# Kernel tuning notes

Hardware: AMD Instinct MI355X
Metric: run time of the kernel (lower is better)

The kernel has to match this reference:

```python
import jax, jax.numpy as jnp
import numpy as np

ALPHA = 0.5
TEMP = 0.1
TEMP2 = 0.05  # hardcoded in nt_xent_loss2
NUM_CLASSES = 10
EPS = 1e-12


def setup_inputs() -> dict:
    key = jax.random.key(0)
    k1, k2, k3 = jax.random.split(key, 3)
    B, D, C = 4096, 256, NUM_CLASSES
    cls_feats = jax.random.normal(k1, (B, D), dtype=jnp.float32)
    predicts = jax.random.normal(k2, (B, C), dtype=jnp.float32)
    targets = jax.random.randint(k3, (B,), 0, C)
    return {"cls_feats": cls_feats, "predicts": predicts, "targets": targets}


def _nt_xent_loss(feats, labels):
    B = feats.shape[0]
    eye = jnp.eye(B, dtype=bool)
    same = labels[:, None] == labels[None, :]
    mask = (same & ~eye).astype(feats.dtype)            # positives, no diagonal
    s = jnp.einsum('bd,cd->bc', feats, feats) / TEMP     # [B,B]
    s = jnp.where(eye, 0.0, s)                           # subtract diag_embed(diag)
    logits = s - jax.lax.stop_gradient(jnp.max(s, axis=1, keepdims=True))
    log_denom = jnp.log(jnp.sum(jnp.exp(logits), axis=1, keepdims=True) + EPS)
    log_prob = logits * mask - log_denom
    mask_sum = jnp.sum(mask, axis=1)
    mask_sum = jnp.where(mask_sum == 0, 1.0, mask_sum)
    pos_logits = jnp.sum(mask * log_prob, axis=1) / mask_sum
    return -jnp.mean(pos_logits)


def _nt_xent_loss2(feats, labels):
    B = feats.shape[0]
    eye = jnp.eye(B, dtype=bool)
    same = labels[:, None] == labels[None, :]
    mask = (same & ~eye).astype(feats.dtype)
    diff = ~same                                         # mask2 / different-label pairs
    S = (feats @ feats.T) / TEMP2                        # [B,B]
    val = jnp.where(diff, S, 0.0)                        # dot * different_label_mask

    # The torch loop body depends only on labels[i] -> compute once per class.
    def per_class(c):
        neg = labels != c                                # negatives of class c
        in_sub = neg[:, None] & neg[None, :]             # submatrix membership
        # row max over columns restricted to the negative set
        maxdot = jnp.max(jnp.where(neg[None, :], val, -jnp.inf), axis=1)  # [B]
        shifted = jnp.where(in_sub, val - maxdot[:, None], -jnp.inf)
        s_c = jnp.sum(jnp.exp(shifted))                  # exp_terms.sum()
        n_c = jnp.sum(jnp.where(in_sub, diff, False).astype(jnp.float32))
        return s_c, n_c

    sums, counts = jax.lax.map(jax.checkpoint(per_class), jnp.arange(NUM_CLASSES))
    x = sums[labels]                                     # [B] negtive_dot_negtive_sum
    negsum = counts[labels]                              # [B]
    all_zero = jnp.all(negsum == 0)
    x = jnp.where(all_zero, x, x / negsum)
    log_prob_row = -jnp.log(x + EPS)                     # constant across each row
    mask_sum = jnp.sum(mask, axis=1)
    mask_sum_safe = jnp.where(mask_sum == 0, 1.0, mask_sum)
    pos_logits = (mask_sum * log_prob_row) / mask_sum_safe
    return -jnp.mean(pos_logits)


def reference(cls_feats, predicts, targets):
    norm = jnp.maximum(jnp.linalg.norm(cls_feats, axis=-1, keepdims=True), EPS)
    feats = cls_feats / norm                             # F.normalize(dim=-1)
    logp = jax.nn.log_softmax(predicts, axis=-1)
    ce = -jnp.mean(jnp.take_along_axis(logp, targets[:, None], axis=1)[:, 0])
    cl = _nt_xent_loss(feats, targets)
    tl = _nt_xent_loss2(feats, targets)
    return (1.0 - ALPHA) * ce + ALPHA * cl + 0.5 * ALPHA * tl
```

## Files before the change

kernel.cpp:

```cpp
#include <hip/hip_runtime.h>
#include <math.h>

#define B 4096
#define D 256
#define NC 10
#define LDW 65
#define ZERO4 22528

typedef __attribute__((ext_vector_type(8))) short bf16x8;
typedef __attribute__((ext_vector_type(4))) float f32x4;

__device__ __forceinline__ unsigned short f2bf(float x) {
    unsigned int u = __float_as_uint(x);
    u += 0x7FFFu + ((u >> 16) & 1u);
    return (unsigned short)(u >> 16);
}

__global__ void scatter_kernel(const float* __restrict__ feats, const float* __restrict__ pred,
                               const int* __restrict__ tg, int* __restrict__ labelP,
                               unsigned short* __restrict__ fP, int* __restrict__ h,
                               float* __restrict__ ceP, float* __restrict__ D1,
                               float4* __restrict__ bigz, float* __restrict__ sums,
                               float* __restrict__ scal, int* __restrict__ done) {
    __shared__ int wcntS[4][NC], wpreS[4][NC];
    __shared__ int allS[NC], preS[NC], cbS[NC];
    __shared__ int posS[64];
    const int t = threadIdx.x, w = t >> 6, l = t & 63;
    const int bid = blockIdx.x, r0 = bid * 64;

    {
        int zi = bid * 352 + t;
        bigz[zi] = (float4){0.f, 0.f, 0.f, 0.f};
        if (t < 96) bigz[zi + 256] = (float4){0.f, 0.f, 0.f, 0.f};
    }
    if (bid == 0) {
        if (t < 16) sums[t] = 0.f;
        else if (t < 32) scal[t - 16] = 0.f;
        else if (t == 32) *done = 0;
    }

    int wc[NC], wp[NC];
#pragma unroll
    for (int c = 0; c < NC; c++) { wc[c] = 0; wp[c] = 0; }
    for (int r = 0; r < 16; ++r) {
        int lab = tg[w * 1024 + r * 64 + l];
        bool blw = (w * 16 + r) < bid;
#pragma unroll
        for (int c = 0; c < NC; c++) {
            int p = __popcll(__ballot(lab == c));
            wc[c] += p;
            wp[c] += blw ? p : 0;
        }
    }
    if (l == 0) {
#pragma unroll
        for (int c = 0; c < NC; c++) { wcntS[w][c] = wc[c]; wpreS[w][c] = wp[c]; }
    }
    __syncthreads();
    if (t < NC) {
        int all = 0, pre = 0;
#pragma unroll
        for (int ww = 0; ww < 4; ww++) { all += wcntS[ww][t]; pre += wpreS[ww][t]; }
        allS[t] = all;
        preS[t] = pre;
        if (bid == 0) h[t] = all;
    }
    __syncthreads();
    if (t < NC) {
        int b = 0;
#pragma unroll
        for (int cc = 0; cc < NC; cc++) b += (cc < t) ? allS[cc] : 0;
        cbS[t] = b;
    }
    __syncthreads();

    if (t < 64) {
        const int lab0 = tg[r0 + t];
        unsigned long long below = (t == 0) ? 0ull : ((~0ull) >> (64 - t));
        int rank = 0;
#pragma unroll
        for (int c = 0; c < NC; c++) {
            unsigned long long m = __ballot(lab0 == c);
            if (lab0 == c) rank = __popcll(m & below);
        }
        int pos = cbS[lab0] + preS[lab0] + rank;
        labelP[pos] = lab0;
        posS[t] = pos;
        const float* p = pred + (r0 + t) * NC;
        float m = p[0];
#pragma unroll
        for (int c = 1; c < NC; c++) m = fmaxf(m, p[c]);
        float s = 0.f;
#pragma unroll
        for (int c = 0; c < NC; c++) s += __expf(p[c] - m);
        float vce = m + logf(s) - p[lab0];
#pragma unroll
        for (int o = 1; o < 64; o <<= 1) vce += __shfl_xor(vce, o);
        if (t == 0) ceP[bid] = vce;
    }
    __syncthreads();

    const int gid = t >> 4, lg = t & 15;
#pragma unroll
    for (int it = 0; it < 4; ++it) {
        const int r = it * 16 + gid;
        float4 v[4];
#pragma unroll
        for (int k = 0; k < 4; k++) v[k] = ((const float4*)feats)[(r0 + r) * 64 + lg * 4 + k];
        float ss = 0.f;
#pragma unroll
        for (int k = 0; k < 4; k++)
            ss += v[k].x * v[k].x + v[k].y * v[k].y + v[k].z * v[k].z + v[k].w * v[k].w;
#pragma unroll
        for (int o = 1; o < 16; o <<= 1) ss += __shfl_xor(ss, o);
        float inv = 1.0f / fmaxf(sqrtf(ss), 1e-12f);
        bf16x8 o0, o1;
#pragma unroll
        for (int k = 0; k < 4; k++) {
            const float* vp = (const float*)&v[k];
            if (k < 2) {
#pragma unroll
                for (int e = 0; e < 4; e++) o0[k * 4 + e] = (short)f2bf(vp[e] * inv);
            } else {
#pragma unroll
                for (int e = 0; e < 4; e++) o1[(k - 2) * 4 + e] = (short)f2bf(vp[e] * inv);
            }
        }
        float gss = 0.f;
#pragma unroll
        for (int e = 0; e < 8; e++) {
            float f0 = __uint_as_float(((unsigned)(unsigned short)o0[e]) << 16);
            float f1 = __uint_as_float(((unsigned)(unsigned short)o1[e]) << 16);
            gss += f0 * f0 + f1 * f1;
        }
#pragma unroll
        for (int o = 1; o < 16; o <<= 1) gss += __shfl_xor(gss, o);
        const int dst = posS[r];
        ((bf16x8*)fP)[dst * 32 + lg * 2 + 0] = o0;
        ((bf16x8*)fP)[dst * 32 + lg * 2 + 1] = o1;
        if (lg == 0) D1[dst] = gss;
    }
}

__launch_bounds__(256)
__global__ void gemm_kernel(const unsigned short* __restrict__ fP,
                            const int* __restrict__ labP,
                            float* __restrict__ E1, float* __restrict__ P1,
                            float* __restrict__ E2G, int* __restrict__ M2K) {
    __shared__ float scW[4][16 * LDW];
    __shared__ int labS[256];
    __shared__ float E2L[32 * 11];
    __shared__ int M2L[32 * 11];
    __shared__ float E1L[32], P1L[32];

    const int t = threadIdx.x;
    const int w = t >> 6, l = t & 63;
    const int qr = l >> 4, lm = l & 15;
    const int row0 = blockIdx.x * 32;
    const int colB = blockIdx.y * 256;

    labS[t] = labP[colB + t];
    for (int s = t; s < 32 * 11; s += 256) { E2L[s] = 0.f; M2L[s] = 0; }
    if (t < 32) { E1L[t] = 0.f; P1L[t] = 0.f; }

    int liR[2];
#pragma unroll
    for (int mb = 0; mb < 2; mb++) liR[mb] = labP[row0 + mb * 16 + lm];

    const unsigned short* pa = fP + (row0 + lm) * D + qr * 8;
    const unsigned short* pb = fP + (colB + w * 64 + lm) * D + qr * 8;

    f32x4 acc[2][4];
#pragma unroll
    for (int mb = 0; mb < 2; mb++)
#pragma unroll
        for (int nb = 0; nb < 4; nb++) acc[mb][nb] = (f32x4){0.f, 0.f, 0.f, 0.f};

#pragma unroll 2
    for (int ks = 0; ks < 8; ks++) {
        bf16x8 af[2], bfr[4];
#pragma unroll
        for (int mb = 0; mb < 2; mb++) af[mb] = *(const bf16x8*)(pa + mb * 16 * D + ks * 32);
#pragma unroll
        for (int nb = 0; nb < 4; nb++) bfr[nb] = *(const bf16x8*)(pb + nb * 16 * D + ks * 32);
#pragma unroll
        for (int mb = 0; mb < 2; mb++)
#pragma unroll
            for (int nb = 0; nb < 4; nb++)
                acc[mb][nb] = __builtin_amdgcn_mfma_f32_16x16x32_bf16(af[mb], bfr[nb],
                                                                      acc[mb][nb], 0, 0, 0);
    }
    __syncthreads();

#pragma unroll
    for (int mb = 0; mb < 2; mb++) {
#pragma unroll
        for (int nb = 0; nb < 4; nb++)
#pragma unroll
            for (int r = 0; r < 4; r++)
                scW[w][(qr * 4 + r) * LDW + nb * 16 + lm] = acc[mb][nb][r];
        const int rowL = mb * 16 + lm;
        const int li = liR[mb];
        const float* srow = &scW[w][lm * LDW + qr * 16];
        float e1sumA = 0.f, e1sumB = 0.f, p1sum = 0.f;
        int seg = -1; float segEA = 0.f, segEB = 0.f; int segK = 0;
#pragma unroll
        for (int j = 0; j < 16; j++) {
            float g = srow[j];
            int lj = labS[w * 64 + qr * 16 + j];
            float g10 = 10.f * g;
            float e1 = __expf(g10);
            if (j & 1) e1sumB += e1; else e1sumA += e1;
            p1sum += (lj == li) ? g : 0.f;
            if (lj != seg) {
                if (seg >= 0) {
                    atomicAdd(&E2L[rowL * 11 + seg], segEA + segEB);
                    atomicMax(&M2L[rowL * 11 + seg], segK);
                }
                seg = lj; segEA = 0.f; segEB = 0.f; segK = 0;
            }
            float e2 = e1 * e1;
            if (j & 1) segEB += e2; else segEA += e2;
            segK = max(segK, __float_as_int(fmaf(2.f, g10, 64.f)));
        }
        atomicAdd(&E2L[rowL * 11 + seg], segEA + segEB);
        atomicMax(&M2L[rowL * 11 + seg], segK);
        float e1sum = e1sumA + e1sumB;
        e1sum += __shfl_xor(e1sum, 16); e1sum += __shfl_xor(e1sum, 32);
        p1sum += __shfl_xor(p1sum, 16); p1sum += __shfl_xor(p1sum, 32);
        if (qr == 0) {
            atomicAdd(&E1L[rowL], e1sum);
            atomicAdd(&P1L[rowL], p1sum * 10.f);
        }
    }
    __syncthreads();

    if (t < 32) {
        atomicAdd(&E1[row0 + t], E1L[t]);
        atomicAdd(&P1[row0 + t], P1L[t]);
    }
    for (int s = t; s < 32 * NC; s += 256) {
        int r = s / NC, c = s - r * NC;
        float e = E2L[r * 11 + c];
        int k = M2L[r * 11 + c];
        if (e > 0.f) atomicAdd(&E2G[(row0 + r) * NC + c], e);
        if (k > 0) atomicMax(&M2K[(row0 + r) * NC + c], k);
    }
}

__global__ void rowfin_kernel(const int* __restrict__ labP, const int* __restrict__ h,
                              const float* __restrict__ E1, const float* __restrict__ P1,
                              const float* __restrict__ E2G, const int* __restrict__ M2K,
                              const float* __restrict__ ceP, const float* __restrict__ D1,
                              float* __restrict__ sums, float* __restrict__ scal,
                              int* __restrict__ done, float* __restrict__ out) {
    __shared__ int lastS;
    const int t = threadIdx.x;
    const int i = blockIdx.x * 64 + t;
    const int li = labP[i];
    float E2[NC], M2[NC];
#pragma unroll
    for (int k = 0; k < NC; k++) {
        E2[k] = E2G[i * NC + k];
        int key = M2K[i * NC + k];
        M2[k] = (key > 0) ? (__int_as_float(key) - 64.f) : -3.0e38f;
    }
    const int hl = h[li];
    E2[li] = (float)hl;
    M2[li] = 0.f;
    float m1 = -3.0e38f, m2 = -3.0e38f;
    int a1 = -1;
#pragma unroll
    for (int k = 0; k < NC; k++) {
        float v = M2[k];
        if (v > m1) { m2 = m1; m1 = v; a1 = k; }
        else if (v > m2) m2 = v;
    }
    float Es = 0.f;
#pragma unroll
    for (int k = 0; k < NC; k++) Es += E2[k];
    float contrib[NC];
#pragma unroll
    for (int c = 0; c < NC; c++) {
        float T = Es - E2[c];
        float md = (a1 == c) ? m2 : m1;
        contrib[c] = (c != li && T > 0.f) ? __expf(-md) * T : 0.f;
    }
#pragma unroll
    for (int c = 0; c < NC; c++) {
        float v = contrib[c];
#pragma unroll
        for (int o = 1; o < 64; o <<= 1) v += __shfl_xor(v, o);
        if (t == 0 && v > 0.f) atomicAdd(&sums[c], v);
    }
    const float gii = D1[i];
    const float E1v = E1[i] + 1.f - __expf(10.f * gii);
    const float P1v = P1[i] - 10.f * gii;
    float cn = (float)(hl - 1);
    float pos1 = (cn > 0.f) ? (P1v / cn - logf(E1v)) : 0.f;
#pragma unroll
    for (int o = 1; o < 64; o <<= 1) pos1 += __shfl_xor(pos1, o);
    if (t == 0) atomicAdd(&scal[1], pos1);

    __threadfence();
    if (t == 0) lastS = (atomicAdd(done, 1) == 63);
    __syncthreads();
    if (lastS && t == 0) {
        int hh[NC];
        long long S2 = 0;
        for (int c = 0; c < NC; c++) { hh[c] = h[c]; S2 += (long long)hh[c] * hh[c]; }
        float ncs[NC];
        int az = 1;
        for (int c = 0; c < NC; c++) {
            long long M = (long long)B - hh[c];
            long long n = M * M - (S2 - (long long)hh[c] * hh[c]);
            ncs[c] = (float)n;
            if (hh[c] > 0 && n != 0) az = 0;
        }
        float possum = 0.f;
        for (int c = 0; c < NC; c++) {
            if (hh[c] > 1) {
                float x = atomicAdd(&sums[c], 0.f);
                if (!az) x = x / ncs[c];
                possum += (float)hh[c] * (-logf(x + 1e-12f));
            }
        }
        float cesum = 0.f;
        for (int b = 0; b < 64; b++) cesum += ceP[b];
        float ce = cesum / (float)B;
        float cl = -(atomicAdd(&scal[1], 0.f) / (float)B);
        float tl = -(possum / (float)B);
        float loss = 0.5f * ce + 0.5f * cl + 0.25f * tl;
        unsigned int bits = __float_as_uint(loss);
        unsigned int hedged = (bits & 0xFFFF0000u) | (bits >> 16);
        *(unsigned int*)out = hedged;
    }
}

extern "C" void kernel_launch(void* const* d_in, const int* in_sizes, int n_in,
                              void* d_out, int out_size, void* d_ws, size_t ws_size,
                              hipStream_t stream) {
    (void)in_sizes; (void)n_in; (void)out_size; (void)ws_size;
    const float* feats = (const float*)d_in[0];
    const float* pred = (const float*)d_in[1];
    const int* tg = (const int*)d_in[2];
    float* out = (float*)d_out;

    unsigned short* fP = (unsigned short*)d_ws;
    float* E1 = (float*)(fP + B * D);
    float* P1 = E1 + B;
    float* E2G = P1 + B;
    int* M2K = (int*)(E2G + B * NC);
    int* h = M2K + B * NC;
    float* ceP = (float*)(h + 16);
    float* sums = ceP + 64;
    float* scal = sums + 16;
    int* done = (int*)(scal + 16);
    int* labelP = done + 16;
    float* D1 = (float*)(labelP + B);

    scatter_kernel<<<64, 256, 0, stream>>>(feats, pred, tg, labelP, fP, h, ceP, D1,
                                           (float4*)E1, sums, scal, done);
    gemm_kernel<<<dim3(B / 32, B / 256), 256, 0, stream>>>(fP, labelP, E1, P1, E2G, M2K);
    rowfin_kernel<<<64, 64, 0, stream>>>(labelP, h, E1, P1, E2G, M2K, ceP, D1,
                                         sums, scal, done, out);
}
```

Before: 135.4 us.

## Fuse row finalization into GEMM kernel via last-block reduction

Removes the separate rowfin kernel launch: the last GEMM block, found with an atomic counter over 2048 blocks, does the per-row finalization for all 4096 rows and the final loss reduction in shared memory, with no global sums or scal atomics. The scatter kernel also preloads its label values into registers before the ballot loop. This saves one launch and its gap, but puts the whole finalization on a single 256-thread block at the tail of the GEMM.

```diff
diff --git a/kernel.cpp b/kernel.cpp
--- a/kernel.cpp
+++ b/kernel.cpp
@@ -20,8 +20,7 @@
                                const int* __restrict__ tg, int* __restrict__ labelP,
                                unsigned short* __restrict__ fP, int* __restrict__ h,
                                float* __restrict__ ceP, float* __restrict__ D1,
-                               float4* __restrict__ bigz, float* __restrict__ sums,
-                               float* __restrict__ scal, int* __restrict__ done) {
+                               float4* __restrict__ bigz, int* __restrict__ done) {
     __shared__ int wcntS[4][NC], wpreS[4][NC];
     __shared__ int allS[NC], preS[NC], cbS[NC];
     __shared__ int posS[64];
@@ -33,21 +32,20 @@
         bigz[zi] = (float4){0.f, 0.f, 0.f, 0.f};
         if (t < 96) bigz[zi + 256] = (float4){0.f, 0.f, 0.f, 0.f};
     }
-    if (bid == 0) {
-        if (t < 16) sums[t] = 0.f;
-        else if (t < 32) scal[t - 16] = 0.f;
-        else if (t == 32) *done = 0;
-    }
-
+    if (bid == 0 && t == 0) *done = 0;
+
+    int labs[16];
+#pragma unroll
+    for (int r = 0; r < 16; ++r) labs[r] = tg[w * 1024 + r * 64 + l];
     int wc[NC], wp[NC];
 #pragma unroll
     for (int c = 0; c < NC; c++) { wc[c] = 0; wp[c] = 0; }
+#pragma unroll
     for (int r = 0; r < 16; ++r) {
-        int lab = tg[w * 1024 + r * 64 + l];
         bool blw = (w * 16 + r) < bid;
 #pragma unroll
         for (int c = 0; c < NC; c++) {
-            int p = __popcll(__ballot(lab == c));
+            int p = __popcll(__ballot(labs[r] == c));
             wc[c] += p;
             wp[c] += blw ? p : 0;
         }
@@ -146,12 +144,20 @@
 __global__ void gemm_kernel(const unsigned short* __restrict__ fP,
                             const int* __restrict__ labP,
                             float* __restrict__ E1, float* __restrict__ P1,
-                            float* __restrict__ E2G, int* __restrict__ M2K) {
+                            float* __restrict__ E2G, int* __restrict__ M2K,
+                            const float* __restrict__ ceP, const float* __restrict__ D1,
+                            const int* __restrict__ h, int* __restrict__ done,
+                            float* __restrict__ out) {
     __shared__ float scW[4][16 * LDW];
     __shared__ int labS[256];
     __shared__ float E2L[32 * 11];
     __shared__ int M2L[32 * 11];
     __shared__ float E1L[32], P1L[32];
+    __shared__ int lastS;
+    __shared__ int hS[NC];
+    __shared__ float wS[4][NC];
+    __shared__ float p1S[4];
+    __shared__ float ceS;
 
     const int t = threadIdx.x;
     const int w = t >> 6, l = t & 63;
@@ -246,69 +252,78 @@
         if (e > 0.f) atomicAdd(&E2G[(row0 + r) * NC + c], e);
         if (k > 0) atomicMax(&M2K[(row0 + r) * NC + c], k);
     }
-}
-
-__global__ void rowfin_kernel(const int* __restrict__ labP, const int* __restrict__ h,
-                              const float* __restrict__ E1, const float* __restrict__ P1,
-                              const float* __restrict__ E2G, const int* __restrict__ M2K,
-                              const float* __restrict__ ceP, const float* __restrict__ D1,
-                              float* __restrict__ sums, float* __restrict__ scal,
-                              int* __restrict__ done, float* __restrict__ out) {
-    __shared__ int lastS;
-    const int t = threadIdx.x;
-    const int i = blockIdx.x * 64 + t;
-    const int li = labP[i];
-    float E2[NC], M2[NC];
-#pragma unroll
-    for (int k = 0; k < NC; k++) {
-        E2[k] = E2G[i * NC + k];
-        int key = M2K[i * NC + k];
-        M2[k] = (key > 0) ? (__int_as_float(key) - 64.f) : -3.0e38f;
-    }
-    const int hl = h[li];
-    E2[li] = (float)hl;
-    M2[li] = 0.f;
-    float m1 = -3.0e38f, m2 = -3.0e38f;
-    int a1 = -1;
-#pragma unroll
-    for (int k = 0; k < NC; k++) {
-        float v = M2[k];
-        if (v > m1) { m2 = m1; m1 = v; a1 = k; }
-        else if (v > m2) m2 = v;
-    }
-    float Es = 0.f;
-#pragma unroll
-    for (int k = 0; k < NC; k++) Es += E2[k];
-    float contrib[NC];
+
+    __threadfence();
+    if (t == 0) lastS = (atomicAdd(done, 1) == 2047);
+    __syncthreads();
+    if (!lastS) return;
+    __threadfence();
+
+    if (t < NC) hS[t] = h[t];
+    __syncthreads();
+
+    float sumsL[NC];
+#pragma unroll
+    for (int c = 0; c < NC; c++) sumsL[c] = 0.f;
+    float pos1a = 0.f;
+#pragma unroll 4
+    for (int it = 0; it < 16; ++it) {
+        const int i = it * 256 + t;
+        const int li = labP[i];
+        const int hl = hS[li];
+        float E2[NC], M2[NC];
+#pragma unroll
+        for (int k = 0; k < NC; k++) {
+            float e2v = E2G[i * NC + k];
+            int key = M2K[i * NC + k];
+            float m2v = (key > 0) ? (__int_as_float(key) - 64.f) : -3.0e38f;
+            E2[k] = (k == li) ? (float)hl : e2v;
+            M2[k] = (k == li) ? 0.f : m2v;
+        }
+        float m1 = -3.0e38f, m2 = -3.0e38f;
+        int a1 = -1;
+#pragma unroll
+        for (int k = 0; k < NC; k++) {
+            float v = M2[k];
+            if (v > m1) { m2 = m1; m1 = v; a1 = k; }
+            else if (v > m2) m2 = v;
+        }
+        float Es = 0.f;
+#pragma unroll
+        for (int k = 0; k < NC; k++) Es += E2[k];
+#pragma unroll
+        for (int c = 0; c < NC; c++) {
+            float T = Es - E2[c];
+            float md = (a1 == c) ? m2 : m1;
+            sumsL[c] += (c != li && T > 0.f) ? __expf(-md) * T : 0.f;
+        }
+        const float gii = D1[i];
+        const float E1v = E1[i] + 1.f - __expf(10.f * gii);
+        const float P1v = P1[i] - 10.f * gii;
+        float cn = (float)(hl - 1);
+        pos1a += (cn > 0.f) ? (P1v / cn - logf(E1v)) : 0.f;
+    }
 #pragma unroll
     for (int c = 0; c < NC; c++) {
-        float T = Es - E2[c];
-        float md = (a1 == c) ? m2 : m1;
-        contrib[c] = (c != li && T > 0.f) ? __expf(-md) * T : 0.f;
-    }
-#pragma unroll
-    for (int c = 0; c < NC; c++) {
-        float v = contrib[c];
+        float v = sumsL[c];
 #pragma unroll
         for (int o = 1; o < 64; o <<= 1) v += __shfl_xor(v, o);
-        if (t == 0 && v > 0.f) atomicAdd(&sums[c], v);
-    }
-    const float gii = D1[i];
-    const float E1v = E1[i] + 1.f - __expf(10.f * gii);
-    const float P1v = P1[i] - 10.f * gii;
-    float cn = (float)(hl - 1);
-    float pos1 = (cn > 0.f) ? (P1v / cn - logf(E1v)) : 0.f;
-#pragma unroll
-    for (int o = 1; o < 64; o <<= 1) pos1 += __shfl_xor(pos1, o);
-    if (t == 0) atomicAdd(&scal[1], pos1);
-
-    __threadfence();
-    if (t == 0) lastS = (atomicAdd(done, 1) == 63);
-    __syncthreads();
-    if (lastS && t == 0) {
+        if (l == 0) wS[w][c] = v;
+    }
+#pragma unroll
+    for (int o = 1; o < 64; o <<= 1) pos1a += __shfl_xor(pos1a, o);
+    if (l == 0) p1S[w] = pos1a;
+    if (t < 64) {
+        float v = ceP[t];
+#pragma unroll
+        for (int o = 1; o < 64; o <<= 1) v += __shfl_xor(v, o);
+        if (t == 0) ceS = v;
+    }
+    __syncthreads();
+    if (t == 0) {
         int hh[NC];
         long long S2 = 0;
-        for (int c = 0; c < NC; c++) { hh[c] = h[c]; S2 += (long long)hh[c] * hh[c]; }
+        for (int c = 0; c < NC; c++) { hh[c] = hS[c]; S2 += (long long)hh[c] * hh[c]; }
         float ncs[NC];
         int az = 1;
         for (int c = 0; c < NC; c++) {
@@ -320,15 +335,13 @@
         float possum = 0.f;
         for (int c = 0; c < NC; c++) {
             if (hh[c] > 1) {
-                float x = atomicAdd(&sums[c], 0.f);
+                float x = wS[0][c] + wS[1][c] + wS[2][c] + wS[3][c];
                 if (!az) x = x / ncs[c];
                 possum += (float)hh[c] * (-logf(x + 1e-12f));
             }
         }
-        float cesum = 0.f;
-        for (int b = 0; b < 64; b++) cesum += ceP[b];
-        float ce = cesum / (float)B;
-        float cl = -(atomicAdd(&scal[1], 0.f) / (float)B);
+        float ce = ceS / (float)B;
+        float cl = -((p1S[0] + p1S[1] + p1S[2] + p1S[3]) / (float)B);
         float tl = -(possum / (float)B);
         float loss = 0.5f * ce + 0.5f * cl + 0.25f * tl;
         unsigned int bits = __float_as_uint(loss);
@@ -353,15 +366,12 @@
     int* M2K = (int*)(E2G + B * NC);
     int* h = M2K + B * NC;
     float* ceP = (float*)(h + 16);
-    float* sums = ceP + 64;
-    float* scal = sums + 16;
-    int* done = (int*)(scal + 16);
+    int* done = (int*)(ceP + 64);
     int* labelP = done + 16;
     float* D1 = (float*)(labelP + B);
 
     scatter_kernel<<<64, 256, 0, stream>>>(feats, pred, tg, labelP, fP, h, ceP, D1,
-                                           (float4*)E1, sums, scal, done);
-    gemm_kernel<<<dim3(B / 32, B / 256), 256, 0, stream>>>(fP, labelP, E1, P1, E2G, M2K);
-    rowfin_kernel<<<64, 64, 0, stream>>>(labelP, h, E1, P1, E2G, M2K, ceP, D1,
-                                         sums, scal, done, out);
+                                           (float4*)E1, done);
+    gemm_kernel<<<dim3(B / 32, B / 256), 256, 0, stream>>>(fP, labelP, E1, P1, E2G, M2K,
+                                                           ceP, D1, h, done, out);
 }
```

Result: slower. 271.1 us (+100.2%).

## Shrink GEMM blocks to one wave and drop the block-level LDS reductions

Applied to the files above, without the earlier changes.

The similarity GEMM now runs one 64-thread wave per block over a 32x64 tile instead of four waves over 32x256. This gives four times as many blocks and removes the block-wide barriers. Per-row E1/P1 partials now go straight to global atomics instead of through an LDS reduction, and each block flushes its per-class E2/M2 partials covering only 64 columns. That raises the number of global atomics roughly fourfold. The scatter kernel also preloads its labels into registers before the ballot loop. Zeroing of sums and scal moves to a separate hipMemsetAsync, which adds one extra operation on the stream.

```diff
diff --git a/kernel.cpp b/kernel.cpp
--- a/kernel.cpp
+++ b/kernel.cpp
@@ -20,8 +20,7 @@
                                const int* __restrict__ tg, int* __restrict__ labelP,
                                unsigned short* __restrict__ fP, int* __restrict__ h,
                                float* __restrict__ ceP, float* __restrict__ D1,
-                               float4* __restrict__ bigz, float* __restrict__ sums,
-                               float* __restrict__ scal, int* __restrict__ done) {
+                               float4* __restrict__ bigz, int* __restrict__ done) {
     __shared__ int wcntS[4][NC], wpreS[4][NC];
     __shared__ int allS[NC], preS[NC], cbS[NC];
     __shared__ int posS[64];
@@ -33,21 +32,20 @@
         bigz[zi] = (float4){0.f, 0.f, 0.f, 0.f};
         if (t < 96) bigz[zi + 256] = (float4){0.f, 0.f, 0.f, 0.f};
     }
-    if (bid == 0) {
-        if (t < 16) sums[t] = 0.f;
-        else if (t < 32) scal[t - 16] = 0.f;
-        else if (t == 32) *done = 0;
-    }
-
+    if (bid == 0 && t == 0) *done = 0;
+
+    int labs[16];
+#pragma unroll
+    for (int r = 0; r < 16; ++r) labs[r] = tg[w * 1024 + r * 64 + l];
     int wc[NC], wp[NC];
 #pragma unroll
     for (int c = 0; c < NC; c++) { wc[c] = 0; wp[c] = 0; }
+#pragma unroll
     for (int r = 0; r < 16; ++r) {
-        int lab = tg[w * 1024 + r * 64 + l];
         bool blw = (w * 16 + r) < bid;
 #pragma unroll
         for (int c = 0; c < NC; c++) {
-            int p = __popcll(__ballot(lab == c));
+            int p = __popcll(__ballot(labs[r] == c));
             wc[c] += p;
             wp[c] += blw ? p : 0;
         }
@@ -142,33 +140,30 @@
     }
 }
 
-__launch_bounds__(256)
+__launch_bounds__(64)
 __global__ void gemm_kernel(const unsigned short* __restrict__ fP,
                             const int* __restrict__ labP,
                             float* __restrict__ E1, float* __restrict__ P1,
                             float* __restrict__ E2G, int* __restrict__ M2K) {
-    __shared__ float scW[4][16 * LDW];
-    __shared__ int labS[256];
+    __shared__ float scW[16 * LDW];
+    __shared__ int labS[64];
     __shared__ float E2L[32 * 11];
     __shared__ int M2L[32 * 11];
-    __shared__ float E1L[32], P1L[32];
 
     const int t = threadIdx.x;
-    const int w = t >> 6, l = t & 63;
-    const int qr = l >> 4, lm = l & 15;
+    const int qr = t >> 4, lm = t & 15;
     const int row0 = blockIdx.x * 32;
-    const int colB = blockIdx.y * 256;
-
-    labS[t] = labP[colB + t];
-    for (int s = t; s < 32 * 11; s += 256) { E2L[s] = 0.f; M2L[s] = 0; }
-    if (t < 32) { E1L[t] = 0.f; P1L[t] = 0.f; }
+    const int col0 = blockIdx.y * 64;
+
+    labS[t] = labP[col0 + t];
+    for (int s = t; s < 32 * 11; s += 64) { E2L[s] = 0.f; M2L[s] = 0; }
 
     int liR[2];
 #pragma unroll
     for (int mb = 0; mb < 2; mb++) liR[mb] = labP[row0 + mb * 16 + lm];
 
     const unsigned short* pa = fP + (row0 + lm) * D + qr * 8;
-    const unsigned short* pb = fP + (colB + w * 64 + lm) * D + qr * 8;
+    const unsigned short* pb = fP + (col0 + lm) * D + qr * 8;
 
     f32x4 acc[2][4];
 #pragma unroll
@@ -190,7 +185,6 @@
                 acc[mb][nb] = __builtin_amdgcn_mfma_f32_16x16x32_bf16(af[mb], bfr[nb],
                                                                       acc[mb][nb], 0, 0, 0);
     }
-    __syncthreads();
 
 #pragma unroll
     for (int mb = 0; mb < 2; mb++) {
@@ -198,16 +192,16 @@
         for (int nb = 0; nb < 4; nb++)
 #pragma unroll
             for (int r = 0; r < 4; r++)
-                scW[w][(qr * 4 + r) * LDW + nb * 16 + lm] = acc[mb][nb][r];
+                scW[(qr * 4 + r) * LDW + nb * 16 + lm] = acc[mb][nb][r];
         const int rowL = mb * 16 + lm;
         const int li = liR[mb];
-        const float* srow = &scW[w][lm * LDW + qr * 16];
+        const float* srow = &scW[lm * LDW + qr * 16];
         float e1sumA = 0.f, e1sumB = 0.f, p1sum = 0.f;
         int seg = -1; float segEA = 0.f, segEB = 0.f; int segK = 0;
 #pragma unroll
         for (int j = 0; j < 16; j++) {
             float g = srow[j];
-            int lj = labS[w * 64 + qr * 16 + j];
+            int lj = labS[qr * 16 + j];
             float g10 = 10.f * g;
             float e1 = __expf(g10);
             if (j & 1) e1sumB += e1; else e1sumA += e1;
@@ -229,17 +223,11 @@
         e1sum += __shfl_xor(e1sum, 16); e1sum += __shfl_xor(e1sum, 32);
         p1sum += __shfl_xor(p1sum, 16); p1sum += __shfl_xor(p1sum, 32);
         if (qr == 0) {
-            atomicAdd(&E1L[rowL], e1sum);
-            atomicAdd(&P1L[rowL], p1sum * 10.f);
-        }
-    }
-    __syncthreads();
-
-    if (t < 32) {
-        atomicAdd(&E1[row0 + t], E1L[t]);
-        atomicAdd(&P1[row0 + t], P1L[t]);
-    }
-    for (int s = t; s < 32 * NC; s += 256) {
+            atomicAdd(&E1[row0 + rowL], e1sum);
+            atomicAdd(&P1[row0 + rowL], p1sum * 10.f);
+        }
+    }
+    for (int s = t; s < 32 * NC; s += 64) {
         int r = s / NC, c = s - r * NC;
         float e = E2L[r * 11 + c];
         int k = M2L[r * 11 + c];
@@ -359,9 +347,11 @@
     int* labelP = done + 16;
     float* D1 = (float*)(labelP + B);
 
+    hipMemsetAsync(sums, 0, 32 * sizeof(float), stream);
+
     scatter_kernel<<<64, 256, 0, stream>>>(feats, pred, tg, labelP, fP, h, ceP, D1,
-                                           (float4*)E1, sums, scal, done);
-    gemm_kernel<<<dim3(B / 32, B / 256), 256, 0, stream>>>(fP, labelP, E1, P1, E2G, M2K);
+                                           (float4*)E1, done);
+    gemm_kernel<<<dim3(B / 32, B / 64), 64, 0, stream>>>(fP, labelP, E1, P1, E2G, M2K);
     rowfin_kernel<<<64, 64, 0, stream>>>(labelP, h, E1, P1, E2G, M2K, ceP, D1,
                                          sums, scal, done, out);
 }
```

After: 141.2 us. 1.04x slower.
